# Optimization experiments

Measured on AMD Instinct MI355X. Metric: run time of the kernel, lower is better.

The kernel has to match this reference:

```python
import jax, jax.numpy as jnp
import numpy as np

B, S, D, H, W = 4, 4096, 1024, 16, 128
HD = D // H


def setup_inputs() -> dict:
    key = jax.random.key(0)
    ks = jax.random.split(key, 12)
    s = 1.0 / np.sqrt(D)
    return {
        "query": jax.random.normal(ks[0], (B, S, D), jnp.float32),
        "key": jax.random.normal(ks[1], (B, S, D), jnp.float32),
        "value": jax.random.normal(ks[2], (B, S, D), jnp.float32),
        "Wq": jax.random.normal(ks[3], (D, D), jnp.float32) * s,
        "bq": jnp.zeros((D,), jnp.float32),
        "Wk": jax.random.normal(ks[4], (D, D), jnp.float32) * s,
        "bk": jnp.zeros((D,), jnp.float32),
        "Wv": jax.random.normal(ks[5], (D, D), jnp.float32) * s,
        "bv": jnp.zeros((D,), jnp.float32),
        "Wo": jax.random.normal(ks[6], (D, D), jnp.float32) * s,
        "bo": jnp.zeros((D,), jnp.float32),
        "global_indices": jnp.arange(32, dtype=jnp.int32),
    }


def _mha(q, k, v, Wq, bq, Wk, bk, Wv, bv, Wo, bo):
    # q,k,v: [..., S, D]; full multi-head attention over the last-but-one axis.
    def split(x):
        return x.reshape(x.shape[:-1] + (H, HD))
    qh = split(q @ Wq.T + bq)
    kh = split(k @ Wk.T + bk)
    vh = split(v @ Wv.T + bv)
    scale = 1.0 / np.sqrt(HD)
    scores = jnp.einsum('...qhd,...khd->...hqk', qh, kh) * scale
    attn = jax.nn.softmax(scores, axis=-1)
    out = jnp.einsum('...hqk,...khd->...qhd', attn, vh)
    out = out.reshape(q.shape)
    return out @ Wo.T + bo


def reference(query, key, value, Wq, bq, Wk, bk, Wv, bv, Wo, bo, global_indices):
    nW = S // W
    # non-overlapping windowed attention: [B, nW, W, D]
    qw = query.reshape(B, nW, W, D)
    kw = key.reshape(B, nW, W, D)
    vw = value.reshape(B, nW, W, D)
    local = _mha(qw, kw, vw, Wq, bq, Wk, bk, Wv, bv, Wo, bo).reshape(B, S, D)
    # global-token pass: attention among global tokens only
    gq = query[:, global_indices]
    gk = key[:, global_indices]
    gv = value[:, global_indices]
    gout = _mha(gq, gk, gv, Wq, bq, Wk, bk, Wv, bv, Wo, bo)
    return local.at[:, global_indices].set(gout)
```

## Files before the change

kernel.cpp:

```cpp
#include <hip/hip_runtime.h>

#define DB 4
#define SS 4096
#define DD 1024
#define HH 16
#define HD 64
#define WW 128
#define NW 32
#define NG 32

typedef __bf16 bf16_t;
typedef bf16_t bf16x4 __attribute__((ext_vector_type(4)));
typedef bf16_t bf16x8 __attribute__((ext_vector_type(8)));
typedef float f32x4 __attribute__((ext_vector_type(4)));

typedef const __attribute__((address_space(1))) void* gptr_t;
typedef __attribute__((address_space(3))) void* lptr_t;

static __device__ __forceinline__ f32x4 mfma16(bf16x8 a, bf16x8 b, f32x4 c) {
    return __builtin_amdgcn_mfma_f32_16x16x32_bf16(a, b, c, 0, 0, 0);
}

__global__ void detect_dtype(const unsigned short* __restrict__ q, int* __restrict__ flag) {
    int lane = threadIdx.x;
    unsigned short u = q[2 * lane];
    bf16_t b;
    __builtin_memcpy(&b, &u, 2);
    float v = fabsf((float)b);
    bool ok = (v > 1e-5f) && (v < 1e5f);
    unsigned long long m = __ballot(ok);
    if (lane == 0) *flag = (__popcll(m) >= 32) ? 1 : 0;
}

__global__ void cvt_x(const void* __restrict__ src, bf16_t* __restrict__ dst,
                      const int* __restrict__ flag) {
    int i = blockIdx.x * blockDim.x + threadIdx.x;
    int e = i * 4;
    if (*flag) {
        *(ushort4*)(dst + e) = ((const ushort4*)src)[i];
    } else {
        float4 f = ((const float4*)src)[i];
        bf16x4 o = { (bf16_t)f.x, (bf16_t)f.y, (bf16_t)f.z, (bf16_t)f.w };
        *(bf16x4*)(dst + e) = o;
    }
}

__global__ void cvt_w(const void* __restrict__ src, bf16_t* __restrict__ wp,
                      const int* __restrict__ flag) {
    int i = blockIdx.x * blockDim.x + threadIdx.x;
    int e = i * 4;
    int n = e >> 10, k = e & 1023;
    int dst = n * 2048 + ((k >> 5) << 6) + (k & 31);
    if (*flag) {
        *(ushort4*)(wp + dst) = ((const ushort4*)src)[i];
        ushort4 z = {0, 0, 0, 0};
        *(ushort4*)(wp + dst + 32) = z;
    } else {
        float4 f = ((const float4*)src)[i];
        bf16x4 h = { (bf16_t)f.x, (bf16_t)f.y, (bf16_t)f.z, (bf16_t)f.w };
        bf16x4 l = { (bf16_t)(f.x - (float)h[0]), (bf16_t)(f.y - (float)h[1]),
                     (bf16_t)(f.z - (float)h[2]), (bf16_t)(f.w - (float)h[3]) };
        *(bf16x4*)(wp + dst) = h;
        *(bf16x4*)(wp + dst + 32) = l;
    }
}

__global__ void cvt_bias(const void* b0, const void* b1, const void* b2, const void* b3,
                         float* __restrict__ dst, const int* __restrict__ flag) {
    int i = blockIdx.x * blockDim.x + threadIdx.x;
    const void* s = (i >> 10) == 0 ? b0 : (i >> 10) == 1 ? b1 : (i >> 10) == 2 ? b2 : b3;
    int j = i & 1023;
    dst[i] = (*flag) ? (float)((const bf16_t*)s)[j] : ((const float*)s)[j];
}

__global__ void expand_out(const bf16_t* __restrict__ src, void* __restrict__ dst,
                           const int* __restrict__ flag) {
    int i = blockIdx.x * blockDim.x + threadIdx.x;
    int e = i * 4;
    ushort4 u = *(const ushort4*)(src + e);
    if (*flag) {
        ((ushort4*)dst)[i] = u;
    } else {
        const bf16x4 b = *(const bf16x4*)&u;
        float4 f = { (float)b[0], (float)b[1], (float)b[2], (float)b[3] };
        ((float4*)dst)[i] = f;
    }
}

#define GFENCE() asm volatile("" ::: "memory")
#define MIDBAR() do { GFENCE(); __builtin_amdgcn_s_barrier(); GFENCE(); } while (0)
#define ENDBAR(N) do { asm volatile("s_waitcnt vmcnt(" #N ")" ::: "memory"); \
                       __builtin_amdgcn_s_barrier(); GFENCE(); } while (0)

#define QUAD_MFMA(MS, NS, BB)                                                          \
    do {                                                                               \
        __builtin_amdgcn_s_setprio(1);                                                 \
        _Pragma("unroll")                                                              \
        for (int t_ = 0; t_ < 4; ++t_) {                                               \
            _Pragma("unroll")                                                          \
            for (int u_ = 0; u_ < 2; ++u_) {                                           \
                acc[(MS)*4 + t_][(NS)*2 + u_] =                                        \
                    mfma16(a[t_][0], BB[u_][0], acc[(MS)*4 + t_][(NS)*2 + u_]);        \
                acc[(MS)*4 + t_][(NS)*2 + u_] =                                        \
                    mfma16(a[t_][1], BB[u_][1], acc[(MS)*4 + t_][(NS)*2 + u_]);        \
            }                                                                          \
        }                                                                              \
        __builtin_amdgcn_s_setprio(0);                                                 \
    } while (0)

__global__ __launch_bounds__(512, 2) void gemm8(const bf16_t* __restrict__ X,
                                                const bf16_t* __restrict__ Wp,
                                                const float* __restrict__ bias,
                                                bf16_t* __restrict__ Y) {
    __shared__ alignas(16) bf16_t sA[2][16384];
    __shared__ alignas(16) bf16_t sB[2][16384];

    const int tid  = threadIdx.x;
    const int lane = tid & 63;
    const int wv   = tid >> 6;
    const int c    = lane & 15;
    const int quad = lane >> 4;
    const int wi   = wv >> 2;
    const int wj   = wv & 3;

    int wg = blockIdx.x;
    wg = (wg & 7) * 32 + (wg >> 3);
    const int mbase = (wg >> 2) * 256;
    const int nbase = (wg & 3) * 256;

    const int d0   = tid * 16;
    const int srow = d0 >> 7;
    const int scol = (d0 & 127) ^ ((srow & 7) << 4);
    const char* srcA = (const char*)X + (size_t)(mbase + srow) * 2048 + (scol & 63);
    const char* srcB = (const char*)Wp +
        (size_t)(nbase + ((srow >> 5) << 6) + (srow & 31)) * 4096 + scol;
    char* const ldsA = (char*)&sA[0][0] + wv * 1024;
    char* const ldsB = (char*)&sB[0][0] + wv * 1024;

    f32x4 acc[8][4] = {};
    const int colX = (quad * 16) ^ ((c & 7) << 4);

    auto stageA = [&](int P, int chunk, int ktb) {
        const char* s0 = srcA + ktb + chunk * 131072;
        char* l0 = ldsA + P * 32768 + chunk * 16384;
        __builtin_amdgcn_global_load_lds((gptr_t)s0,            (lptr_t)l0,          16, 0, 0);
        __builtin_amdgcn_global_load_lds((gptr_t)(s0 + 262144), (lptr_t)(l0 + 8192), 16, 0, 0);
    };
    auto stageB = [&](int P, int chunk, int ktb) {
        const char* s0 = srcB + ktb + chunk * 131072;
        char* l0 = ldsB + P * 32768 + chunk * 16384;
        __builtin_amdgcn_global_load_lds((gptr_t)s0,            (lptr_t)l0,          16, 0, 0);
        __builtin_amdgcn_global_load_lds((gptr_t)(s0 + 524288), (lptr_t)(l0 + 8192), 16, 0, 0);
    };

    bf16x8 a[4][2], b0[2][2], b1[2][2];

    auto ldA = [&](int P, int ms) {
        const char* base = (const char*)&sA[0][0] + P * 32768 +
                           (size_t)(ms * 128 + wi * 64 + c) * 128;
        #pragma unroll
        for (int t = 0; t < 4; ++t) {
            a[t][0] = *(const bf16x8*)(base + t * 2048 + colX);
            a[t][1] = *(const bf16x8*)(base + t * 2048 + (colX ^ 64));
        }
    };
    auto ldB0 = [&](int P) {
        const char* base = (const char*)&sB[0][0] + P * 32768 +
                           (size_t)(wj * 32 + c) * 128;
        #pragma unroll
        for (int u = 0; u < 2; ++u) {
            b0[u][0] = *(const bf16x8*)(base + u * 2048 + colX);
            b0[u][1] = *(const bf16x8*)(base + u * 2048 + (colX ^ 64));
        }
    };
    auto ldB1 = [&](int P) {
        const char* base = (const char*)&sB[0][0] + P * 32768 + 16384 +
                           (size_t)(wj * 32 + c) * 128;
        #pragma unroll
        for (int u = 0; u < 2; ++u) {
            b1[u][0] = *(const bf16x8*)(base + u * 2048 + colX);
            b1[u][1] = *(const bf16x8*)(base + u * 2048 + (colX ^ 64));
        }
    };

    stageA(0, 0, 0); stageB(0, 0, 0);
    stageA(0, 1, 0); stageB(0, 1, 0);
    ENDBAR(4);

    int kA = 64, kB = 128;
    for (int t = 0; t < 31; ++t) {
        const int P = t & 1, Q = P ^ 1;
        ldA(P, 0); ldB0(P);
        stageA(Q, 0, kA);
        MIDBAR();
        QUAD_MFMA(0, 0, b0);
        ENDBAR(2);
        ldB1(P);
        stageB(Q, 0, kB);
        MIDBAR();
        QUAD_MFMA(0, 1, b1);
        MIDBAR();
        ldA(P, 1);
        stageA(Q, 1, kA);
        MIDBAR();
        QUAD_MFMA(1, 1, b1);
        MIDBAR();
        stageB(Q, 1, kB);
        MIDBAR();
        QUAD_MFMA(1, 0, b0);
        ENDBAR(4);
        kA += 64; kB += 128;
    }
    ENDBAR(0);
    ldA(1, 0); ldB0(1); ldB1(1);
    QUAD_MFMA(0, 0, b0);
    QUAD_MFMA(0, 1, b1);
    ldA(1, 1);
    QUAD_MFMA(1, 1, b1);
    QUAD_MFMA(1, 0, b0);

    #pragma unroll
    for (int n = 0; n < 4; ++n) {
        const int col = nbase + wj * 64 + (n >> 1) * 32 + (n & 1) * 16 + c;
        const float bv = bias[col];
        #pragma unroll
        for (int m = 0; m < 8; ++m) {
            const int row = mbase + wi * 128 + (m >> 2) * 64 + (m & 3) * 16 + quad * 4;
            #pragma unroll
            for (int r = 0; r < 4; ++r)
                Y[(size_t)(row + r) * DD + col] = (bf16_t)(acc[m][n][r] + bv);
        }
    }
}

__global__ __launch_bounds__(256) void attn_local(const bf16_t* __restrict__ Q,
                                                  const bf16_t* __restrict__ K,
                                                  const bf16_t* __restrict__ V,
                                                  bf16_t* __restrict__ ctx) {
    const int wx = blockIdx.x, h = blockIdx.y, b = blockIdx.z;
    const int tid  = threadIdx.x;
    const int lane = tid & 63;
    const int wv   = tid >> 6;
    const int c    = lane & 15;
    const int quad = lane >> 4;

    __shared__ alignas(16) bf16_t pbuf[128][136];
    __shared__ alignas(16) bf16_t vtb[64][136];

    const size_t base = ((size_t)b * SS + (size_t)wx * WW) * DD + (size_t)h * HD;

    for (int e = tid; e < WW * HD; e += 256) {
        int j = e >> 6, d = e & 63;
        vtb[d][j] = V[base + (size_t)j * DD + d];
    }

    const float scale = 0.125f;

    #pragma unroll
    for (int ii = 0; ii < 2; ++ii) {
        const int it = wv * 2 + ii;
        f32x4 s[8] = {};
        #pragma unroll
        for (int kt = 0; kt < 2; ++kt) {
            bf16x8 a = *(const bf16x8*)(Q + base + (size_t)(it * 16 + c) * DD + kt * 32 + quad * 8);
            #pragma unroll
            for (int jt = 0; jt < 8; ++jt) {
                bf16x8 bb = *(const bf16x8*)(K + base + (size_t)(jt * 16 + c) * DD + kt * 32 + quad * 8);
                s[jt] = mfma16(a, bb, s[jt]);
            }
        }
        #pragma unroll
        for (int jt = 0; jt < 8; ++jt) s[jt] *= scale;

        #pragma unroll
        for (int r = 0; r < 4; ++r) {
            float m = -1e30f;
            #pragma unroll
            for (int jt = 0; jt < 8; ++jt) m = fmaxf(m, s[jt][r]);
            #pragma unroll
            for (int off = 1; off < 16; off <<= 1) m = fmaxf(m, __shfl_xor(m, off));
            float p[8], sum = 0.f;
            #pragma unroll
            for (int jt = 0; jt < 8; ++jt) { p[jt] = __expf(s[jt][r] - m); sum += p[jt]; }
            #pragma unroll
            for (int off = 1; off < 16; off <<= 1) sum += __shfl_xor(sum, off);
            float inv = 1.0f / sum;
            int row = it * 16 + quad * 4 + r;
            #pragma unroll
            for (int jt = 0; jt < 8; ++jt) pbuf[row][jt * 16 + c] = (bf16_t)(p[jt] * inv);
        }
    }

    __syncthreads();

    #pragma unroll
    for (int ii = 0; ii < 2; ++ii) {
        const int it = wv * 2 + ii;
        f32x4 o[4] = {};
        #pragma unroll
        for (int kt = 0; kt < 4; ++kt) {
            bf16x8 a = *(const bf16x8*)&pbuf[it * 16 + c][kt * 32 + quad * 8];
            #pragma unroll
            for (int dt = 0; dt < 4; ++dt) {
                bf16x8 bb = *(const bf16x8*)&vtb[dt * 16 + c][kt * 32 + quad * 8];
                o[dt] = mfma16(a, bb, o[dt]);
            }
        }
        #pragma unroll
        for (int dt = 0; dt < 4; ++dt)
            #pragma unroll
            for (int r = 0; r < 4; ++r)
                ctx[base + (size_t)(it * 16 + quad * 4 + r) * DD + dt * 16 + c] = (bf16_t)(o[dt][r]);
    }
}

__global__ __launch_bounds__(256) void attn_global(const bf16_t* __restrict__ Q,
                                                   const bf16_t* __restrict__ K,
                                                   const bf16_t* __restrict__ V,
                                                   const int* __restrict__ gidx,
                                                   bf16_t* __restrict__ ctx) {
    const int h = blockIdx.x, b = blockIdx.y;
    const int tid = threadIdx.x;

    __shared__ float qs[NG][HD], ks[NG][HD], vs[NG][HD];
    __shared__ float sc[NG][NG + 1];
    __shared__ int gi[NG];

    if (tid < NG) gi[tid] = gidx[tid];
    __syncthreads();

    for (int e = tid; e < NG * HD; e += 256) {
        int i = e >> 6, d = e & 63;
        size_t off = ((size_t)b * SS + gi[i]) * DD + (size_t)h * HD + d;
        qs[i][d] = (float)Q[off];
        ks[i][d] = (float)K[off];
        vs[i][d] = (float)V[off];
    }
    __syncthreads();

    for (int e = tid; e < NG * NG; e += 256) {
        int i = e >> 5, j = e & 31;
        float s = 0.f;
        #pragma unroll 8
        for (int d = 0; d < HD; ++d) s += qs[i][d] * ks[j][d];
        sc[i][j] = s * 0.125f;
    }
    __syncthreads();

    if (tid < NG) {
        float m = -1e30f;
        for (int j = 0; j < NG; ++j) m = fmaxf(m, sc[tid][j]);
        float sum = 0.f;
        for (int j = 0; j < NG; ++j) { float p = __expf(sc[tid][j] - m); sc[tid][j] = p; sum += p; }
        float inv = 1.f / sum;
        for (int j = 0; j < NG; ++j) sc[tid][j] *= inv;
    }
    __syncthreads();

    for (int e = tid; e < NG * HD; e += 256) {
        int i = e >> 6, d = e & 63;
        float o = 0.f;
        #pragma unroll 8
        for (int j = 0; j < NG; ++j) o += sc[i][j] * vs[j][d];
        ctx[((size_t)b * SS + gi[i]) * DD + (size_t)h * HD + d] = (bf16_t)o;
    }
}

extern "C" void kernel_launch(void* const* d_in, const int* in_sizes, int n_in,
                              void* d_out, int out_size, void* d_ws, size_t ws_size,
                              hipStream_t stream) {
    const void* query = d_in[0];
    const void* key_  = d_in[1];
    const void* value = d_in[2];
    const void* Wq = d_in[3];  const void* bq = d_in[4];
    const void* Wk = d_in[5];  const void* bk = d_in[6];
    const void* Wv = d_in[7];  const void* bv = d_in[8];
    const void* Wo = d_in[9];  const void* bo = d_in[10];
    const int* gidx = (const int*)d_in[11];

    const size_t nTok = (size_t)DB * SS * DD;
    const size_t nW   = (size_t)DD * DD;

    int*    flag    = (int*)d_ws;
    float*  biasbuf = (float*)((char*)d_ws + 256);
    bf16_t* Xh      = (bf16_t*)((char*)d_ws + 32768);
    bf16_t* Qp      = Xh + nTok;
    bf16_t* Kp      = Qp + nTok;
    bf16_t* Ybf     = Xh;

    bf16_t* Wlo  = (bf16_t*)d_out;
    bf16_t* ctx  = (bf16_t*)d_out;
    bf16_t* Vp   = (bf16_t*)d_out + nTok;
    bf16_t* Whi  = Vp;

    detect_dtype<<<1, 64, 0, stream>>>((const unsigned short*)query, flag);
    cvt_bias<<<16, 256, 0, stream>>>(bq, bk, bv, bo, biasbuf, flag);

    cvt_w<<<1024, 256, 0, stream>>>(Wq, Wlo, flag);
    cvt_x<<<16384, 256, 0, stream>>>(query, Xh, flag);
    gemm8<<<256, 512, 0, stream>>>(Xh, Wlo, biasbuf + 0, Qp);

    cvt_w<<<1024, 256, 0, stream>>>(Wk, Wlo, flag);
    cvt_x<<<16384, 256, 0, stream>>>(key_, Xh, flag);
    gemm8<<<256, 512, 0, stream>>>(Xh, Wlo, biasbuf + 1024, Kp);

    cvt_w<<<1024, 256, 0, stream>>>(Wv, Wlo, flag);
    cvt_x<<<16384, 256, 0, stream>>>(value, Xh, flag);
    gemm8<<<256, 512, 0, stream>>>(Xh, Wlo, biasbuf + 2048, Vp);

    attn_local<<<dim3(NW, HH, DB), 256, 0, stream>>>(Qp, Kp, Vp, ctx);
    attn_global<<<dim3(HH, DB), 256, 0, stream>>>(Qp, Kp, Vp, gidx, ctx);

    cvt_w<<<1024, 256, 0, stream>>>(Wo, Whi, flag);
    gemm8<<<256, 512, 0, stream>>>(ctx, Whi, biasbuf + 3072, Ybf);
    expand_out<<<16384, 256, 0, stream>>>(Ybf, d_out, flag);
}
```

Baseline: 589.6 us.

## Drop split-bf16 weight compensation, halve GEMM K loop, fuse fp32 output write

Result: faster. 505.2 us (-14.3%).

```diff
diff --git a/kernel.cpp b/kernel.cpp
--- a/kernel.cpp
+++ b/kernel.cpp
@@ -49,19 +49,12 @@
                       const int* __restrict__ flag) {
     int i = blockIdx.x * blockDim.x + threadIdx.x;
     int e = i * 4;
-    int n = e >> 10, k = e & 1023;
-    int dst = n * 2048 + ((k >> 5) << 6) + (k & 31);
     if (*flag) {
-        *(ushort4*)(wp + dst) = ((const ushort4*)src)[i];
-        ushort4 z = {0, 0, 0, 0};
-        *(ushort4*)(wp + dst + 32) = z;
+        *(ushort4*)(wp + e) = ((const ushort4*)src)[i];
     } else {
         float4 f = ((const float4*)src)[i];
         bf16x4 h = { (bf16_t)f.x, (bf16_t)f.y, (bf16_t)f.z, (bf16_t)f.w };
-        bf16x4 l = { (bf16_t)(f.x - (float)h[0]), (bf16_t)(f.y - (float)h[1]),
-                     (bf16_t)(f.z - (float)h[2]), (bf16_t)(f.w - (float)h[3]) };
-        *(bf16x4*)(wp + dst) = h;
-        *(bf16x4*)(wp + dst + 32) = l;
+        *(bf16x4*)(wp + e) = h;
     }
 }
 
@@ -71,20 +64,6 @@
     const void* s = (i >> 10) == 0 ? b0 : (i >> 10) == 1 ? b1 : (i >> 10) == 2 ? b2 : b3;
     int j = i & 1023;
     dst[i] = (*flag) ? (float)((const bf16_t*)s)[j] : ((const float*)s)[j];
-}
-
-__global__ void expand_out(const bf16_t* __restrict__ src, void* __restrict__ dst,
-                           const int* __restrict__ flag) {
-    int i = blockIdx.x * blockDim.x + threadIdx.x;
-    int e = i * 4;
-    ushort4 u = *(const ushort4*)(src + e);
-    if (*flag) {
-        ((ushort4*)dst)[i] = u;
-    } else {
-        const bf16x4 b = *(const bf16x4*)&u;
-        float4 f = { (float)b[0], (float)b[1], (float)b[2], (float)b[3] };
-        ((float4*)dst)[i] = f;
-    }
 }
 
 #define GFENCE() asm volatile("" ::: "memory")
@@ -111,7 +90,9 @@
 __global__ __launch_bounds__(512, 2) void gemm8(const bf16_t* __restrict__ X,
                                                 const bf16_t* __restrict__ Wp,
                                                 const float* __restrict__ bias,
-                                                bf16_t* __restrict__ Y) {
+                                                void* __restrict__ Yout,
+                                                const int* __restrict__ flag,
+                                                int final_out) {
     __shared__ alignas(16) bf16_t sA[2][16384];
     __shared__ alignas(16) bf16_t sB[2][16384];
 
@@ -123,6 +104,8 @@
     const int wi   = wv >> 2;
     const int wj   = wv & 3;
 
+    const int f32out = final_out ? (*flag == 0) : 0;
+
     int wg = blockIdx.x;
     wg = (wg & 7) * 32 + (wg >> 3);
     const int mbase = (wg >> 2) * 256;
@@ -131,9 +114,9 @@
     const int d0   = tid * 16;
     const int srow = d0 >> 7;
     const int scol = (d0 & 127) ^ ((srow & 7) << 4);
-    const char* srcA = (const char*)X + (size_t)(mbase + srow) * 2048 + (scol & 63);
+    const char* srcA = (const char*)X + (size_t)(mbase + srow) * 2048 + scol;
     const char* srcB = (const char*)Wp +
-        (size_t)(nbase + ((srow >> 5) << 6) + (srow & 31)) * 4096 + scol;
+        (size_t)(nbase + ((srow >> 5) << 6) + (srow & 31)) * 2048 + scol;
     char* const ldsA = (char*)&sA[0][0] + wv * 1024;
     char* const ldsB = (char*)&sB[0][0] + wv * 1024;
 
@@ -147,10 +130,10 @@
         __builtin_amdgcn_global_load_lds((gptr_t)(s0 + 262144), (lptr_t)(l0 + 8192), 16, 0, 0);
     };
     auto stageB = [&](int P, int chunk, int ktb) {
-        const char* s0 = srcB + ktb + chunk * 131072;
+        const char* s0 = srcB + ktb + chunk * 65536;
         char* l0 = ldsB + P * 32768 + chunk * 16384;
         __builtin_amdgcn_global_load_lds((gptr_t)s0,            (lptr_t)l0,          16, 0, 0);
-        __builtin_amdgcn_global_load_lds((gptr_t)(s0 + 524288), (lptr_t)(l0 + 8192), 16, 0, 0);
+        __builtin_amdgcn_global_load_lds((gptr_t)(s0 + 262144), (lptr_t)(l0 + 8192), 16, 0, 0);
     };
 
     bf16x8 a[4][2], b0[2][2], b1[2][2];
@@ -187,29 +170,29 @@
     stageA(0, 1, 0); stageB(0, 1, 0);
     ENDBAR(4);
 
-    int kA = 64, kB = 128;
-    for (int t = 0; t < 31; ++t) {
+    int kk = 128;
+    for (int t = 0; t < 15; ++t) {
         const int P = t & 1, Q = P ^ 1;
         ldA(P, 0); ldB0(P);
-        stageA(Q, 0, kA);
+        stageA(Q, 0, kk);
         MIDBAR();
         QUAD_MFMA(0, 0, b0);
         ENDBAR(2);
         ldB1(P);
-        stageB(Q, 0, kB);
+        stageB(Q, 0, kk);
         MIDBAR();
         QUAD_MFMA(0, 1, b1);
         MIDBAR();
         ldA(P, 1);
-        stageA(Q, 1, kA);
+        stageA(Q, 1, kk);
         MIDBAR();
         QUAD_MFMA(1, 1, b1);
         MIDBAR();
-        stageB(Q, 1, kB);
+        stageB(Q, 1, kk);
         MIDBAR();
         QUAD_MFMA(1, 0, b0);
         ENDBAR(4);
-        kA += 64; kB += 128;
+        kk += 128;
     }
     ENDBAR(0);
     ldA(1, 0); ldB0(1); ldB1(1);
@@ -227,8 +210,12 @@
         for (int m = 0; m < 8; ++m) {
             const int row = mbase + wi * 128 + (m >> 2) * 64 + (m & 3) * 16 + quad * 4;
             #pragma unroll
-            for (int r = 0; r < 4; ++r)
-                Y[(size_t)(row + r) * DD + col] = (bf16_t)(acc[m][n][r] + bv);
+            for (int r = 0; r < 4; ++r) {
+                const float yv = acc[m][n][r] + bv;
+                const size_t idx = (size_t)(row + r) * DD + col;
+                if (f32out) ((float*)Yout)[idx] = yv;
+                else        ((bf16_t*)Yout)[idx] = (bf16_t)yv;
+            }
         }
     }
 }
@@ -379,39 +366,36 @@
     const int* gidx = (const int*)d_in[11];
 
     const size_t nTok = (size_t)DB * SS * DD;
-    const size_t nW   = (size_t)DD * DD;
 
     int*    flag    = (int*)d_ws;
     float*  biasbuf = (float*)((char*)d_ws + 256);
     bf16_t* Xh      = (bf16_t*)((char*)d_ws + 32768);
     bf16_t* Qp      = Xh + nTok;
     bf16_t* Kp      = Qp + nTok;
-    bf16_t* Ybf     = Xh;
-
-    bf16_t* Wlo  = (bf16_t*)d_out;
-    bf16_t* ctx  = (bf16_t*)d_out;
-    bf16_t* Vp   = (bf16_t*)d_out + nTok;
-    bf16_t* Whi  = Vp;
+    bf16_t* ctx     = Xh;
+    bf16_t* Wop     = Kp;
+
+    bf16_t* Wlo = (bf16_t*)d_out;
+    bf16_t* Vp  = (bf16_t*)d_out + nTok;
 
     detect_dtype<<<1, 64, 0, stream>>>((const unsigned short*)query, flag);
     cvt_bias<<<16, 256, 0, stream>>>(bq, bk, bv, bo, biasbuf, flag);
 
     cvt_w<<<1024, 256, 0, stream>>>(Wq, Wlo, flag);
     cvt_x<<<16384, 256, 0, stream>>>(query, Xh, flag);
-    gemm8<<<256, 512, 0, stream>>>(Xh, Wlo, biasbuf + 0, Qp);
+    gemm8<<<256, 512, 0, stream>>>(Xh, Wlo, biasbuf + 0, Qp, flag, 0);
 
     cvt_w<<<1024, 256, 0, stream>>>(Wk, Wlo, flag);
     cvt_x<<<16384, 256, 0, stream>>>(key_, Xh, flag);
-    gemm8<<<256, 512, 0, stream>>>(Xh, Wlo, biasbuf + 1024, Kp);
+    gemm8<<<256, 512, 0, stream>>>(Xh, Wlo, biasbuf + 1024, Kp, flag, 0);
 
     cvt_w<<<1024, 256, 0, stream>>>(Wv, Wlo, flag);
     cvt_x<<<16384, 256, 0, stream>>>(value, Xh, flag);
-    gemm8<<<256, 512, 0, stream>>>(Xh, Wlo, biasbuf + 2048, Vp);
+    gemm8<<<256, 512, 0, stream>>>(Xh, Wlo, biasbuf + 2048, Vp, flag, 0);
 
     attn_local<<<dim3(NW, HH, DB), 256, 0, stream>>>(Qp, Kp, Vp, ctx);
     attn_global<<<dim3(HH, DB), 256, 0, stream>>>(Qp, Kp, Vp, gidx, ctx);
 
-    cvt_w<<<1024, 256, 0, stream>>>(Wo, Whi, flag);
-    gemm8<<<256, 512, 0, stream>>>(ctx, Whi, biasbuf + 3072, Ybf);
-    expand_out<<<16384, 256, 0, stream>>>(Ybf, d_out, flag);
-}
+    cvt_w<<<1024, 256, 0, stream>>>(Wo, Wop, flag);
+    gemm8<<<256, 512, 0, stream>>>(ctx, Wop, biasbuf + 3072, d_out, flag, 1);
+}
```
